# Kernel tuning notes

Measured on AMD Instinct MI355X. Metric: run time of the kernel, lower is better.

Reference implementation:

```python
import jax, jax.numpy as jnp
import numpy as np

D_IN = 2048
D_OUT = 2048
NUM_HEADS = 32
NUM_KV_GROUPS = 8
HEAD_DIM = D_OUT // NUM_HEADS          # 64
GROUP_SIZE = NUM_HEADS // NUM_KV_GROUPS  # 4
BATCH = 2
SEQ = 2048


def _rope(x, cos, sin):
    # x: [b, h, s, d]; cos/sin: [s, d]
    d = x.shape[-1]
    x1, x2 = x[..., : d // 2], x[..., d // 2:]
    rotated = jnp.concatenate((-x2, x1), axis=-1)
    return x * cos[None, None, :, :] + rotated * sin[None, None, :, :]


def setup_inputs() -> dict:
    key = jax.random.key(0)
    ks = jax.random.split(key, 8)
    x = jax.random.normal(ks[0], (BATCH, SEQ, D_IN), dtype=jnp.float32)
    cos = jax.random.normal(ks[1], (SEQ, HEAD_DIM), dtype=jnp.float32)
    sin = jax.random.normal(ks[2], (SEQ, HEAD_DIM), dtype=jnp.float32)
    # causal mask: True above the diagonal = masked out
    mask = jnp.triu(jnp.ones((SEQ, SEQ), dtype=jnp.bool_), k=1)
    s = 0.02
    Wq = jax.random.normal(ks[3], (D_IN, D_OUT), dtype=jnp.float32) * s
    Wk = jax.random.normal(ks[4], (D_IN, NUM_KV_GROUPS * HEAD_DIM), dtype=jnp.float32) * s
    Wv = jax.random.normal(ks[5], (D_IN, NUM_KV_GROUPS * HEAD_DIM), dtype=jnp.float32) * s
    Wo = jax.random.normal(ks[6], (D_OUT, D_OUT), dtype=jnp.float32) * s
    return {"x": x, "cos": cos, "sin": sin, "mask": mask,
            "Wq": Wq, "Wk": Wk, "Wv": Wv, "Wo": Wo}


def reference(x, cos, sin, mask, Wq, Wk, Wv, Wo):
    b, s, _ = x.shape
    # projections (Linear, no bias): weights stored as [d_in, d_out]
    q = (x @ Wq).reshape(b, s, NUM_HEADS, HEAD_DIM).transpose(0, 2, 1, 3)      # [b,H,s,d]
    k = (x @ Wk).reshape(b, s, NUM_KV_GROUPS, HEAD_DIM).transpose(0, 2, 1, 3)  # [b,G,s,d]
    v = (x @ Wv).reshape(b, s, NUM_KV_GROUPS, HEAD_DIM).transpose(0, 2, 1, 3)  # [b,G,s,d]
    q = _rope(q, cos, sin)
    k = _rope(k, cos, sin)
    # GQA broadcast: repeat each KV group group_size times along head axis
    k = jnp.repeat(k, GROUP_SIZE, axis=1)  # [b,H,s,d]
    v = jnp.repeat(v, GROUP_SIZE, axis=1)  # [b,H,s,d]
    scores = jnp.einsum('bhqd,bhkd->bhqk', q, k)
    scores = jnp.where(mask[None, None, :, :], -jnp.inf, scores)
    # original scales AFTER masking: softmax(scores / sqrt(head_dim)); -inf stays -inf
    attn = jax.nn.softmax(scores * (1.0 / np.sqrt(HEAD_DIM)), axis=-1)
    ctx = jnp.einsum('bhqk,bhkd->bqhd', attn, v).reshape(b, s, D_OUT)
    return ctx @ Wo
```

## Files before the change

### kernel.cpp

```cpp
#include <hip/hip_runtime.h>
#include <hip/hip_fp16.h>

#define SEQ    2048
#define DIN    2048
#define DOUT   2048
#define NH     32
#define NKV    8
#define HD     64
#define BB     2
#define NT_K   32

typedef _Float16 half_t;
typedef __attribute__((ext_vector_type(8))) _Float16 half8;
typedef __attribute__((ext_vector_type(4))) _Float16 half4;
typedef __attribute__((ext_vector_type(2))) __fp16   fp16x2;
typedef __attribute__((ext_vector_type(4))) float    floatx4;

union H8U { half8 h; int u[4]; };
union H2I { fp16x2 h; int i; };

#if __has_builtin(__builtin_amdgcn_exp2f)
#define EXP2F(x) __builtin_amdgcn_exp2f(x)
#else
#define EXP2F(x) __expf((x) * 0.6931471805599453f)
#endif

__device__ __forceinline__ void gload16(void* l, const void* g) {
    __builtin_amdgcn_global_load_lds(
        (const __attribute__((address_space(1))) void*)g,
        (__attribute__((address_space(3))) void*)l, 16, 0, 0);
}

__device__ __forceinline__ void phase_bar() {
    __builtin_amdgcn_sched_barrier(0);
    __builtin_amdgcn_s_barrier();
    __builtin_amdgcn_sched_barrier(0);
}
#define LGKM0() do { asm volatile("s_waitcnt lgkmcnt(0)" ::: "memory"); \
                     __builtin_amdgcn_sched_barrier(0); } while (0)
#define VMW(n)  do { asm volatile("s_waitcnt vmcnt(" #n ")" ::: "memory"); \
                     __builtin_amdgcn_sched_barrier(0); } while (0)

__global__ void cast_f2h(const float* __restrict__ in, half_t* __restrict__ out, int n4) {
    int i = blockIdx.x * blockDim.x + threadIdx.x;
    if (i < n4) {
        float4 v = ((const float4*)in)[i];
        half4 h;
        h[0] = (half_t)v.x; h[1] = (half_t)v.y; h[2] = (half_t)v.z; h[3] = (half_t)v.w;
        ((half4*)out)[i] = h;
    }
}

__global__ __launch_bounds__(256) void tcast(const float* __restrict__ in, half_t* __restrict__ out,
                                             int Kd, int Nd) {
    __shared__ float T[32][33];
    int x0 = blockIdx.x * 32, y0 = blockIdx.y * 32;
    int tx = threadIdx.x & 31, ty = threadIdx.x >> 5;
    #pragma unroll
    for (int j = 0; j < 4; j++)
        T[ty + j * 8][tx] = in[(size_t)(y0 + ty + j * 8) * Nd + x0 + tx];
    __syncthreads();
    #pragma unroll
    for (int j = 0; j < 4; j++)
        out[(size_t)(x0 + ty + j * 8) * Kd + y0 + tx] = (half_t)T[tx][ty + j * 8];
}

__device__ __forceinline__ void gemm256_core(
    const half_t* __restrict__ A, const half_t* __restrict__ Bt,
    int m0, int n0, half_t* As, half_t* Bs, floatx4 (&acc)[8][4])
{
    const int tid  = threadIdx.x;
    const int wave = tid >> 6, lane = tid & 63;
    const int quad = lane >> 4, l15 = lane & 15;
    const int wr128 = (wave >> 2) * 128, wc64 = (wave & 3) * 64;
    const int K = DIN;

    const half_t* pa[4]; const half_t* pb[4]; int ldso[4];
    #pragma unroll
    for (int is = 0; is < 4; is++) {
        int s  = is * 512 + tid;
        int kb = s >> 10, s1 = s & 1023;
        int p  = s1 >> 3, c = (s1 & 7) ^ (p & 7);
        int row  = 2 * p + (c >> 2);
        int koff = kb * 32 + (c & 3) * 8;
        pa[is] = A  + (size_t)(m0 + row) * K + koff;
        pb[is] = Bt + (size_t)(n0 + row) * K + koff;
        ldso[is] = (is * 512 + wave * 64) * 8;
    }
    int aoff[8], boff[4];
    #pragma unroll
    for (int m = 0; m < 8; m++) {
        int r = wr128 + m * 16 + l15, p = r >> 1;
        aoff[m] = p * 64 + ((((r & 1) * 4 + quad) ^ (p & 7)) * 8);
    }
    #pragma unroll
    for (int n = 0; n < 4; n++) {
        int r = wc64 + n * 16 + l15, p = r >> 1;
        boff[n] = p * 64 + ((((r & 1) * 4 + quad) ^ (p & 7)) * 8);
    }

    #pragma unroll
    for (int is = 0; is < 4; is++) {
        gload16(As + ldso[is], pa[is]);
        gload16(Bs + ldso[is], pb[is]);
    }
    #pragma unroll
    for (int is = 0; is < 4; is++) {
        gload16(As + 16384 + ldso[is], pa[is] + 64);
        gload16(Bs + 16384 + ldso[is], pb[is] + 64);
    }
    VMW(8);
    phase_bar();

    half8 af[4][2], bf[4][2];
    for (int T = 0; T < NT_K; T++) {
        half_t* cA = As + (T & 1) * 16384;
        half_t* cB = Bs + (T & 1) * 16384;

        #pragma unroll
        for (int mi = 0; mi < 4; mi++) {
            af[mi][0] = *(const half8*)(cA + aoff[mi]);
            af[mi][1] = *(const half8*)(cA + 8192 + aoff[mi]);
        }
        #pragma unroll
        for (int ni = 0; ni < 2; ni++) {
            bf[ni][0] = *(const half8*)(cB + boff[ni]);
            bf[ni][1] = *(const half8*)(cB + 8192 + boff[ni]);
        }
        phase_bar();
        LGKM0();
        __builtin_amdgcn_s_setprio(1);
        #pragma unroll
        for (int ni = 0; ni < 2; ni++)
            #pragma unroll
            for (int mi = 0; mi < 4; mi++)
                #pragma unroll
                for (int ks = 0; ks < 2; ks++)
                    acc[mi][ni] = __builtin_amdgcn_mfma_f32_16x16x32_f16(af[mi][ks], bf[ni][ks], acc[mi][ni], 0, 0, 0);
        __builtin_amdgcn_s_setprio(0);
        phase_bar();

        #pragma unroll
        for (int ni = 2; ni < 4; ni++) {
            bf[ni][0] = *(const half8*)(cB + boff[ni]);
            bf[ni][1] = *(const half8*)(cB + 8192 + boff[ni]);
        }
        phase_bar();
        LGKM0();
        __builtin_amdgcn_s_setprio(1);
        #pragma unroll
        for (int ni = 2; ni < 4; ni++)
            #pragma unroll
            for (int mi = 0; mi < 4; mi++)
                #pragma unroll
                for (int ks = 0; ks < 2; ks++)
                    acc[mi][ni] = __builtin_amdgcn_mfma_f32_16x16x32_f16(af[mi][ks], bf[ni][ks], acc[mi][ni], 0, 0, 0);
        __builtin_amdgcn_s_setprio(0);
        phase_bar();

        #pragma unroll
        for (int mi = 0; mi < 4; mi++) {
            af[mi][0] = *(const half8*)(cA + aoff[4 + mi]);
            af[mi][1] = *(const half8*)(cA + 8192 + aoff[4 + mi]);
        }
        phase_bar();
        LGKM0();
        __builtin_amdgcn_s_setprio(1);
        #pragma unroll
        for (int ni = 0; ni < 2; ni++)
            #pragma unroll
            for (int mi = 0; mi < 4; mi++)
                #pragma unroll
                for (int ks = 0; ks < 2; ks++)
                    acc[4 + mi][ni] = __builtin_amdgcn_mfma_f32_16x16x32_f16(af[mi][ks], bf[ni][ks], acc[4 + mi][ni], 0, 0, 0);
        __builtin_amdgcn_s_setprio(0);
        phase_bar();

        if (T + 2 < NT_K) {
            const int kk = (T + 2) * 64;
            #pragma unroll
            for (int is = 0; is < 4; is++) {
                gload16(cA + ldso[is], pa[is] + kk);
                gload16(cB + ldso[is], pb[is] + kk);
            }
            __builtin_amdgcn_s_setprio(1);
            #pragma unroll
            for (int ni = 2; ni < 4; ni++)
                #pragma unroll
                for (int mi = 0; mi < 4; mi++)
                    #pragma unroll
                    for (int ks = 0; ks < 2; ks++)
                        acc[4 + mi][ni] = __builtin_amdgcn_mfma_f32_16x16x32_f16(af[mi][ks], bf[ni][ks], acc[4 + mi][ni], 0, 0, 0);
            __builtin_amdgcn_s_setprio(0);
            VMW(8);
        } else {
            __builtin_amdgcn_s_setprio(1);
            #pragma unroll
            for (int ni = 2; ni < 4; ni++)
                #pragma unroll
                for (int mi = 0; mi < 4; mi++)
                    #pragma unroll
                    for (int ks = 0; ks < 2; ks++)
                        acc[4 + mi][ni] = __builtin_amdgcn_mfma_f32_16x16x32_f16(af[mi][ks], bf[ni][ks], acc[4 + mi][ni], 0, 0, 0);
            __builtin_amdgcn_s_setprio(0);
            VMW(0);
        }
        phase_bar();
    }
}

__global__ __launch_bounds__(512, 2) void gemm_qkv(
    const half_t* __restrict__ A, const half_t* __restrict__ Bt,
    const float* __restrict__ cosb, const float* __restrict__ sinb,
    half_t* __restrict__ Qh, half_t* __restrict__ Kh, half_t* __restrict__ Vt)
{
    __shared__ half_t As[2][16384];
    __shared__ half_t Bs[2][16384];
    const int m0 = blockIdx.y * 256, n0 = blockIdx.x * 256;

    floatx4 acc[8][4] = {};
    gemm256_core(A, Bt, m0, n0, &As[0][0], &Bs[0][0], acc);

    const int tid = threadIdx.x, wave = tid >> 6, lane = tid & 63;
    const int quad = lane >> 4, l15 = lane & 15;
    const int wr128 = (wave >> 2) * 128, wc64 = (wave & 3) * 64;
    const int headg = (n0 + wc64) >> 6;
    const int b = m0 >> 11;
    const int s_base = (m0 & 2047) + wr128 + quad * 4;

    if (headg < 32) {
        half_t* outp = Qh + (size_t)(b * NH + headg) * SEQ * 64;
        #pragma unroll
        for (int m = 0; m < 8; m++)
            #pragma unroll
            for (int n = 0; n < 4; n++) {
                int d = n * 16 + l15;
                #pragma unroll
                for (int r = 0; r < 4; r++)
                    outp[(size_t)(s_base + m * 16 + r) * 64 + d] = (half_t)acc[m][n][r];
            }
    } else if (headg < 40) {
        half_t* outp = Kh + (size_t)(b * NKV + (headg - 32)) * SEQ * 64;
        #pragma unroll
        for (int m = 0; m < 8; m++)
            #pragma unroll
            for (int r = 0; r < 4; r++) {
                int s = s_base + m * 16 + r;
                #pragma unroll
                for (int j = 0; j < 2; j++) {
                    int d = j * 16 + l15;
                    float x1 = acc[m][j][r], x2 = acc[m][j + 2][r];
                    float c1 = cosb[s * 64 + d],      s1 = sinb[s * 64 + d];
                    float c2 = cosb[s * 64 + d + 32], s2 = sinb[s * 64 + d + 32];
                    outp[(size_t)s * 64 + d]      = (half_t)(x1 * c1 - x2 * s1);
                    outp[(size_t)s * 64 + d + 32] = (half_t)(x2 * c2 + x1 * s2);
                }
            }
    } else {
        half_t* vtp = Vt + (size_t)(b * NKV + (headg - 40)) * 64 * SEQ;
        #pragma unroll
        for (int m = 0; m < 8; m++) {
            int s = s_base + m * 16;
            #pragma unroll
            for (int n = 0; n < 4; n++) {
                int d = n * 16 + l15;
                half4 hv;
                hv[0] = (half_t)acc[m][n][0];
                hv[1] = (half_t)acc[m][n][1];
                hv[2] = (half_t)acc[m][n][2];
                hv[3] = (half_t)acc[m][n][3];
                *(half4*)(vtp + (size_t)d * SEQ + s) = hv;
            }
        }
    }
}

__global__ __launch_bounds__(512, 2) void gemm_tn_f(
    const half_t* __restrict__ A, const half_t* __restrict__ Bt,
    float* __restrict__ C)
{
    __shared__ half_t As[2][16384];
    __shared__ half_t Bs[2][16384];
    const int m0 = blockIdx.y * 256, n0 = blockIdx.x * 256;

    floatx4 acc[8][4] = {};
    gemm256_core(A, Bt, m0, n0, &As[0][0], &Bs[0][0], acc);

    const int tid = threadIdx.x, wave = tid >> 6, lane = tid & 63;
    const int quad = lane >> 4, l15 = lane & 15;
    const int wr128 = (wave >> 2) * 128, wc64 = (wave & 3) * 64;
    #pragma unroll
    for (int m = 0; m < 8; m++) {
        int row = m0 + wr128 + m * 16 + quad * 4;
        #pragma unroll
        for (int n = 0; n < 4; n++) {
            int col = n0 + wc64 + n * 16 + l15;
            #pragma unroll
            for (int r = 0; r < 4; r++)
                C[(size_t)(row + r) * DOUT + col] = acc[m][n][r];
        }
    }
}

__global__ __launch_bounds__(256, 4) void attn(
    const half_t* __restrict__ Qh, const half_t* __restrict__ Kh,
    const half_t* __restrict__ Vt, const float* __restrict__ cosb,
    const float* __restrict__ sinb, half_t* __restrict__ ctx)
{
    __shared__ half_t Ks[2][4096];
    __shared__ half_t Vs[2][4096];

    const int tid = threadIdx.x, wave = tid >> 6, lane = tid & 63;
    const int quad = lane >> 4, l15 = lane & 15;
    const int bid = blockIdx.x;
    const int k  = bid >> 8;
    const int u  = bid & 255;
    const int q2 = u & 3;
    const int bh = u >> 2;
    const int qt = (k == 0) ? 15 - 2 * q2 : (k == 1) ? 2 * q2
                 : (k == 2) ? 14 - 2 * q2 : 2 * q2 + 1;
    const int b  = bh >> 5;
    const int h  = bh & 31;
    const int g  = h >> 2;
    const int q0 = qt * 128;
    const int wm = wave * 32;

    const half_t* kp = Kh + (size_t)(b * NKV + g) * SEQ * 64;
    const half_t* vp = Vt + (size_t)(b * NKV + g) * 64 * SEQ;

    half8 qf[2][2];
    {
        const float sc = 0.125f * 1.44269504088896f;
        const half_t* qpp = Qh + ((size_t)(b * NH + h) * SEQ + q0 + wm) * 64;
        #pragma unroll
        for (int mf = 0; mf < 2; mf++) {
            int s = q0 + wm + mf * 16 + l15;
            const float* cp = cosb + s * 64 + quad * 8;
            const float* sp = sinb + s * 64 + quad * 8;
            half8 xa = *(const half8*)(qpp + (size_t)(mf * 16 + l15) * 64 + quad * 8);
            half8 xb = *(const half8*)(qpp + (size_t)(mf * 16 + l15) * 64 + 32 + quad * 8);
            float4 c1a = *(const float4*)(cp),      c1b = *(const float4*)(cp + 4);
            float4 s1a = *(const float4*)(sp),      s1b = *(const float4*)(sp + 4);
            float4 c2a = *(const float4*)(cp + 32), c2b = *(const float4*)(cp + 36);
            float4 s2a = *(const float4*)(sp + 32), s2b = *(const float4*)(sp + 36);
            #pragma unroll
            for (int t = 0; t < 8; t++) {
                float cc1 = (t < 4) ? ((const float*)&c1a)[t] : ((const float*)&c1b)[t - 4];
                float ss1 = (t < 4) ? ((const float*)&s1a)[t] : ((const float*)&s1b)[t - 4];
                float cc2 = (t < 4) ? ((const float*)&c2a)[t] : ((const float*)&c2b)[t - 4];
                float ss2 = (t < 4) ? ((const float*)&s2a)[t] : ((const float*)&s2b)[t - 4];
                float x1 = (float)xa[t], x2 = (float)xb[t];
                qf[mf][0][t] = (half_t)((x1 * cc1 - x2 * ss1) * sc);
                qf[mf][1][t] = (half_t)((x2 * cc2 + x1 * ss2) * sc);
            }
        }
    }

    int koff[2], voff[2], lo[2];
    #pragma unroll
    for (int is = 0; is < 2; is++) {
        int s = is * 256 + tid;
        int p = s >> 3, c = (s & 7) ^ (p & 7);
        koff[is] = p * 64 + c * 8;
        voff[is] = p * SEQ + c * 8;
        lo[is]   = (is * 256 + wave * 64) * 8;
    }

    float m_i[2], l_i[2];
    m_i[0] = m_i[1] = -__builtin_inff();
    l_i[0] = l_i[1] = 0.f;
    floatx4 o[2][4] = {};

    const int ntiles = 2 * qt + 2;
    #pragma unroll
    for (int is = 0; is < 2; is++) {
        gload16(&Ks[0][lo[is]], kp + koff[is]);
        gload16(&Vs[0][lo[is]], vp + voff[is]);
    }

    const int srcA = l15 + ((quad & 1) ? 32 : 0);
    const int srcB = srcA + 16;
    const bool hiK = (quad >> 1) != 0;

    for (int kt = 0; kt < ntiles; kt++) {
        const int cur = kt & 1;
        const int kb  = kt * 64;
        __syncthreads();
        if (kt + 1 < ntiles) {
            const int kb2 = (kt + 1) * 64;
            #pragma unroll
            for (int is = 0; is < 2; is++) {
                gload16(&Ks[cur ^ 1][lo[is]], kp + (size_t)kb2 * 64 + koff[is]);
                gload16(&Vs[cur ^ 1][lo[is]], vp + kb2 + voff[is]);
            }
        }

        if (kb <= q0 + wm + 31) {
            floatx4 sa[2][4] = {};
            #pragma unroll
            for (int kc = 0; kc < 2; kc++)
                #pragma unroll
                for (int kf = 0; kf < 4; kf++) {
                    int row = kf * 16 + l15;
                    int sc = ((kc * 4 + quad) ^ (row & 7));
                    half8 kfr = *(const half8*)&Ks[cur][row * 64 + sc * 8];
                    sa[0][kf] = __builtin_amdgcn_mfma_f32_16x16x32_f16(kfr, qf[0][kc], sa[0][kf], 0, 0, 0);
                    sa[1][kf] = __builtin_amdgcn_mfma_f32_16x16x32_f16(kfr, qf[1][kc], sa[1][kf], 0, 0, 0);
                }

            if (kb + 63 > q0 + wm) {
                #pragma unroll
                for (int kf = 0; kf < 4; kf++)
                    #pragma unroll
                    for (int r = 0; r < 4; r++) {
                        int key = kb + kf * 16 + quad * 4 + r;
                        if (key > q0 + wm + l15)      sa[0][kf][r] = -__builtin_inff();
                        if (key > q0 + wm + 16 + l15) sa[1][kf][r] = -__builtin_inff();
                    }
            }

            int eh[2][4][2];
            float alpha[2];
            #pragma unroll
            for (int mf = 0; mf < 2; mf++) {
                float mt = sa[mf][0][0];
                #pragma unroll
                for (int kf = 0; kf < 4; kf++)
                    #pragma unroll
                    for (int r = 0; r < 4; r++) mt = fmaxf(mt, sa[mf][kf][r]);
                mt = fmaxf(mt, __shfl_xor(mt, 16));
                mt = fmaxf(mt, __shfl_xor(mt, 32));
                float mn = fmaxf(m_i[mf], mt);
                alpha[mf] = EXP2F(m_i[mf] - mn);
                m_i[mf] = mn;
                float rs = 0.f;
                #pragma unroll
                for (int kf = 0; kf < 4; kf++) {
                    float e0 = EXP2F(sa[mf][kf][0] - mn);
                    float e1 = EXP2F(sa[mf][kf][1] - mn);
                    float e2 = EXP2F(sa[mf][kf][2] - mn);
                    float e3 = EXP2F(sa[mf][kf][3] - mn);
                    rs += (e0 + e1) + (e2 + e3);
                    H2I p01, p23;
                    p01.h = __builtin_amdgcn_cvt_pkrtz(e0, e1);
                    p23.h = __builtin_amdgcn_cvt_pkrtz(e2, e3);
                    eh[mf][kf][0] = p01.i;
                    eh[mf][kf][1] = p23.i;
                }
                rs += __shfl_xor(rs, 16);
                rs += __shfl_xor(rs, 32);
                l_i[mf] = l_i[mf] * alpha[mf] + rs;
                #pragma unroll
                for (int nf = 0; nf < 4; nf++)
                    #pragma unroll
                    for (int r = 0; r < 4; r++) o[mf][nf][r] *= alpha[mf];
            }

            #pragma unroll
            for (int kc = 0; kc < 2; kc++) {
                H8U pf[2];
                #pragma unroll
                for (int mf = 0; mf < 2; mf++) {
                    int a0 = __shfl(eh[mf][2 * kc][0],     srcA);
                    int a1 = __shfl(eh[mf][2 * kc][1],     srcA);
                    int b0 = __shfl(eh[mf][2 * kc + 1][0], srcA);
                    int b1 = __shfl(eh[mf][2 * kc + 1][1], srcA);
                    int c0 = __shfl(eh[mf][2 * kc][0],     srcB);
                    int c1 = __shfl(eh[mf][2 * kc][1],     srcB);
                    int d0 = __shfl(eh[mf][2 * kc + 1][0], srcB);
                    int d1 = __shfl(eh[mf][2 * kc + 1][1], srcB);
                    pf[mf].u[0] = hiK ? b0 : a0;
                    pf[mf].u[1] = hiK ? b1 : a1;
                    pf[mf].u[2] = hiK ? d0 : c0;
                    pf[mf].u[3] = hiK ? d1 : c1;
                }
                #pragma unroll
                for (int nf = 0; nf < 4; nf++) {
                    int row = nf * 16 + l15;
                    int sc = ((kc * 4 + quad) ^ (row & 7));
                    half8 vf = *(const half8*)&Vs[cur][row * 64 + sc * 8];
                    o[0][nf] = __builtin_amdgcn_mfma_f32_16x16x32_f16(vf, pf[0].h, o[0][nf], 0, 0, 0);
                    o[1][nf] = __builtin_amdgcn_mfma_f32_16x16x32_f16(vf, pf[1].h, o[1][nf], 0, 0, 0);
                }
            }
        }
    }

    #pragma unroll
    for (int mf = 0; mf < 2; mf++) {
        float inv = 1.0f / l_i[mf];
        int s = q0 + wm + mf * 16 + l15;
        half_t* op = ctx + (size_t)(b * SEQ + s) * DOUT + h * 64 + quad * 4;
        #pragma unroll
        for (int nf = 0; nf < 4; nf++) {
            half4 hv;
            hv[0] = (half_t)(o[mf][nf][0] * inv);
            hv[1] = (half_t)(o[mf][nf][1] * inv);
            hv[2] = (half_t)(o[mf][nf][2] * inv);
            hv[3] = (half_t)(o[mf][nf][3] * inv);
            *(half4*)(op + nf * 16) = hv;
        }
    }
}

extern "C" void kernel_launch(void* const* d_in, const int* in_sizes, int n_in,
                              void* d_out, int out_size, void* d_ws, size_t ws_size,
                              hipStream_t stream) {
    const float* x    = (const float*)d_in[0];
    const float* cosb = (const float*)d_in[1];
    const float* sinb = (const float*)d_in[2];
    const float* Wq   = (const float*)d_in[4];
    const float* Wk   = (const float*)d_in[5];
    const float* Wv   = (const float*)d_in[6];
    const float* Wo   = (const float*)d_in[7];
    float* out = (float*)d_out;

    const size_t M  = (size_t)BB * SEQ;
    const size_t nX = M * DIN;

    char* ws = (char*)d_ws;
    const size_t MB = 1048576;
    half_t* xh     = (half_t*)(ws);
    half_t* WqkvT  = (half_t*)(ws + 16 * MB);
    half_t* WoT    = (half_t*)(ws + 28 * MB);
    half_t* Qh     = (half_t*)(ws + 36 * MB);
    half_t* Kh     = (half_t*)(ws + 52 * MB);
    half_t* Vt     = (half_t*)(ws + 56 * MB);
    half_t* ctxh   = (half_t*)(ws + 60 * MB);

    cast_f2h<<<(nX / 4) / 256, 256, 0, stream>>>(x, xh, nX / 4);
    tcast<<<dim3(64, 64), 256, 0, stream>>>(Wq, WqkvT, DIN, DOUT);
    tcast<<<dim3(16, 64), 256, 0, stream>>>(Wk, WqkvT + (size_t)2048 * 2048, DIN, 512);
    tcast<<<dim3(16, 64), 256, 0, stream>>>(Wv, WqkvT + (size_t)2560 * 2048, DIN, 512);
    tcast<<<dim3(64, 64), 256, 0, stream>>>(Wo, WoT, DOUT, DOUT);

    gemm_qkv<<<dim3(3072 / 256, M / 256), 512, 0, stream>>>(xh, WqkvT, cosb, sinb, Qh, Kh, Vt);

    attn<<<BB * NH * (SEQ / 128), 256, 0, stream>>>(Qh, Kh, Vt, cosb, sinb, ctxh);

    gemm_tn_f<<<dim3(DOUT / 256, M / 256), 512, 0, stream>>>(ctxh, WoT, out);
}
```

Measured before the change: 383.0 us.

## Interleave GEMM global-to-LDS staging across MFMA phases at quarter-tile granularity

Reworks the GEMM main loop so each K-tile's global-to-LDS loads are split into four quarter stages (two A halves, two B halves). Each stage is issued inside a different MFMA phase, and vmcnt is waited at a finer level (vmcnt(2)). The loop is unrolled by two with static buffer pointers, and the sched_barrier fences around barriers and waits are removed. The aim is to spread memory traffic evenly over compute and shorten the time spent waiting on loads. The cost is that correctness now depends on delicate buffer-reuse ordering, and the compiler has more freedom to reorder code across waits.

After: 354.6 us. 1.08x faster.

```diff
diff --git a/kernel.cpp b/kernel.cpp
--- a/kernel.cpp
+++ b/kernel.cpp
@@ -31,15 +31,10 @@
         (__attribute__((address_space(3))) void*)l, 16, 0, 0);
 }
 
-__device__ __forceinline__ void phase_bar() {
-    __builtin_amdgcn_sched_barrier(0);
-    __builtin_amdgcn_s_barrier();
-    __builtin_amdgcn_sched_barrier(0);
-}
-#define LGKM0() do { asm volatile("s_waitcnt lgkmcnt(0)" ::: "memory"); \
-                     __builtin_amdgcn_sched_barrier(0); } while (0)
-#define VMW(n)  do { asm volatile("s_waitcnt vmcnt(" #n ")" ::: "memory"); \
-                     __builtin_amdgcn_sched_barrier(0); } while (0)
+#define BAR()   __builtin_amdgcn_s_barrier()
+#define LGKM0() asm volatile("s_waitcnt lgkmcnt(0)")
+#define VMW2()  asm volatile("s_waitcnt vmcnt(2)" ::: "memory")
+#define VMW0()  asm volatile("s_waitcnt vmcnt(0)" ::: "memory")
 
 __global__ void cast_f2h(const float* __restrict__ in, half_t* __restrict__ out, int n4) {
     int i = blockIdx.x * blockDim.x + threadIdx.x;
@@ -65,9 +60,39 @@
         out[(size_t)(x0 + ty + j * 8) * Kd + y0 + tx] = (half_t)T[tx][ty + j * 8];
 }
 
+#define DS_AQ(Q) \
+    _Pragma("unroll") \
+    for (int mi = 0; mi < 4; mi++) { \
+        af[mi][0] = *(const half8*)(cA + aoff[(Q) + mi]); \
+        af[mi][1] = *(const half8*)(cA + 8192 + aoff[(Q) + mi]); \
+    }
+#define DS_BH(N0, N1) \
+    _Pragma("unroll") \
+    for (int ni = (N0); ni < (N1); ni++) { \
+        bf[ni][0] = *(const half8*)(cB + boff[ni]); \
+        bf[ni][1] = *(const half8*)(cB + 8192 + boff[ni]); \
+    }
+#define MFMA_Q(MI0, NI0) \
+    __builtin_amdgcn_s_setprio(1); \
+    _Pragma("unroll") \
+    for (int ni = 0; ni < 2; ni++) \
+        _Pragma("unroll") \
+        for (int mi = 0; mi < 4; mi++) \
+            _Pragma("unroll") \
+            for (int ks = 0; ks < 2; ks++) \
+                acc[(MI0) + mi][(NI0) + ni] = __builtin_amdgcn_mfma_f32_16x16x32_f16( \
+                    af[mi][ks], bf[(NI0) + ni][ks], acc[(MI0) + mi][(NI0) + ni], 0, 0, 0); \
+    __builtin_amdgcn_s_setprio(0);
+
+#define PH_GROUP(STG0, STG1, STG2, STG3, VMW_) \
+    DS_AQ(0); DS_BH(0, 2); STG0; BAR(); LGKM0(); MFMA_Q(0, 0); BAR(); \
+    DS_BH(2, 4);           STG1; BAR(); LGKM0(); MFMA_Q(0, 2); BAR(); \
+    DS_AQ(4);              STG2; BAR(); LGKM0(); MFMA_Q(4, 0); BAR(); \
+    STG3; MFMA_Q(4, 2); VMW_; BAR();
+
 __device__ __forceinline__ void gemm256_core(
     const half_t* __restrict__ A, const half_t* __restrict__ Bt,
-    int m0, int n0, half_t* As, half_t* Bs, floatx4 (&acc)[8][4])
+    int m0, int n0, half_t* AsB, half_t* BsB, floatx4 (&acc)[8][4])
 {
     const int tid  = threadIdx.x;
     const int wave = tid >> 6, lane = tid & 63;
@@ -99,113 +124,47 @@
         boff[n] = p * 64 + ((((r & 1) * 4 + quad) ^ (p & 7)) * 8);
     }
 
-    #pragma unroll
-    for (int is = 0; is < 4; is++) {
-        gload16(As + ldso[is], pa[is]);
-        gload16(Bs + ldso[is], pb[is]);
-    }
-    #pragma unroll
-    for (int is = 0; is < 4; is++) {
-        gload16(As + 16384 + ldso[is], pa[is] + 64);
-        gload16(Bs + 16384 + ldso[is], pb[is] + 64);
-    }
-    VMW(8);
-    phase_bar();
+    auto stage = [&](int tile, int ht) {
+        const int kk = tile * 64;
+        half_t* dst = (ht < 2 ? AsB : BsB) + (tile & 1) * 16384;
+        const int i0 = (ht & 1) * 2;
+        if (ht < 2) {
+            gload16(dst + ldso[i0],     pa[i0] + kk);
+            gload16(dst + ldso[i0 + 1], pa[i0 + 1] + kk);
+        } else {
+            gload16(dst + ldso[i0],     pb[i0] + kk);
+            gload16(dst + ldso[i0 + 1], pb[i0 + 1] + kk);
+        }
+    };
+
+    stage(0, 0); stage(0, 1); stage(0, 2); stage(0, 3);
+    stage(1, 0);
+    VMW2();
+    BAR();
 
     half8 af[4][2], bf[4][2];
-    for (int T = 0; T < NT_K; T++) {
-        half_t* cA = As + (T & 1) * 16384;
-        half_t* cB = Bs + (T & 1) * 16384;
-
-        #pragma unroll
-        for (int mi = 0; mi < 4; mi++) {
-            af[mi][0] = *(const half8*)(cA + aoff[mi]);
-            af[mi][1] = *(const half8*)(cA + 8192 + aoff[mi]);
-        }
-        #pragma unroll
-        for (int ni = 0; ni < 2; ni++) {
-            bf[ni][0] = *(const half8*)(cB + boff[ni]);
-            bf[ni][1] = *(const half8*)(cB + 8192 + boff[ni]);
-        }
-        phase_bar();
-        LGKM0();
-        __builtin_amdgcn_s_setprio(1);
-        #pragma unroll
-        for (int ni = 0; ni < 2; ni++)
-            #pragma unroll
-            for (int mi = 0; mi < 4; mi++)
-                #pragma unroll
-                for (int ks = 0; ks < 2; ks++)
-                    acc[mi][ni] = __builtin_amdgcn_mfma_f32_16x16x32_f16(af[mi][ks], bf[ni][ks], acc[mi][ni], 0, 0, 0);
-        __builtin_amdgcn_s_setprio(0);
-        phase_bar();
-
-        #pragma unroll
-        for (int ni = 2; ni < 4; ni++) {
-            bf[ni][0] = *(const half8*)(cB + boff[ni]);
-            bf[ni][1] = *(const half8*)(cB + 8192 + boff[ni]);
-        }
-        phase_bar();
-        LGKM0();
-        __builtin_amdgcn_s_setprio(1);
-        #pragma unroll
-        for (int ni = 2; ni < 4; ni++)
-            #pragma unroll
-            for (int mi = 0; mi < 4; mi++)
-                #pragma unroll
-                for (int ks = 0; ks < 2; ks++)
-                    acc[mi][ni] = __builtin_amdgcn_mfma_f32_16x16x32_f16(af[mi][ks], bf[ni][ks], acc[mi][ni], 0, 0, 0);
-        __builtin_amdgcn_s_setprio(0);
-        phase_bar();
-
-        #pragma unroll
-        for (int mi = 0; mi < 4; mi++) {
-            af[mi][0] = *(const half8*)(cA + aoff[4 + mi]);
-            af[mi][1] = *(const half8*)(cA + 8192 + aoff[4 + mi]);
-        }
-        phase_bar();
-        LGKM0();
-        __builtin_amdgcn_s_setprio(1);
-        #pragma unroll
-        for (int ni = 0; ni < 2; ni++)
-            #pragma unroll
-            for (int mi = 0; mi < 4; mi++)
-                #pragma unroll
-                for (int ks = 0; ks < 2; ks++)
-                    acc[4 + mi][ni] = __builtin_amdgcn_mfma_f32_16x16x32_f16(af[mi][ks], bf[ni][ks], acc[4 + mi][ni], 0, 0, 0);
-        __builtin_amdgcn_s_setprio(0);
-        phase_bar();
-
-        if (T + 2 < NT_K) {
-            const int kk = (T + 2) * 64;
-            #pragma unroll
-            for (int is = 0; is < 4; is++) {
-                gload16(cA + ldso[is], pa[is] + kk);
-                gload16(cB + ldso[is], pb[is] + kk);
-            }
-            __builtin_amdgcn_s_setprio(1);
-            #pragma unroll
-            for (int ni = 2; ni < 4; ni++)
-                #pragma unroll
-                for (int mi = 0; mi < 4; mi++)
-                    #pragma unroll
-                    for (int ks = 0; ks < 2; ks++)
-                        acc[4 + mi][ni] = __builtin_amdgcn_mfma_f32_16x16x32_f16(af[mi][ks], bf[ni][ks], acc[4 + mi][ni], 0, 0, 0);
-            __builtin_amdgcn_s_setprio(0);
-            VMW(8);
-        } else {
-            __builtin_amdgcn_s_setprio(1);
-            #pragma unroll
-            for (int ni = 2; ni < 4; ni++)
-                #pragma unroll
-                for (int mi = 0; mi < 4; mi++)
-                    #pragma unroll
-                    for (int ks = 0; ks < 2; ks++)
-                        acc[4 + mi][ni] = __builtin_amdgcn_mfma_f32_16x16x32_f16(af[mi][ks], bf[ni][ks], acc[4 + mi][ni], 0, 0, 0);
-            __builtin_amdgcn_s_setprio(0);
-            VMW(0);
-        }
-        phase_bar();
+    #pragma unroll 1
+    for (int i = 0; i < NT_K / 2 - 1; i++) {
+        const int t0 = 2 * i;
+        {
+            const half_t* cA = AsB; const half_t* cB = BsB;
+            PH_GROUP(stage(t0 + 1, 1), stage(t0 + 1, 2), stage(t0 + 1, 3),
+                     stage(t0 + 2, 0), VMW2());
+        }
+        {
+            const half_t* cA = AsB + 16384; const half_t* cB = BsB + 16384;
+            PH_GROUP(stage(t0 + 2, 1), stage(t0 + 2, 2), stage(t0 + 2, 3),
+                     stage(t0 + 3, 0), VMW2());
+        }
+    }
+    {
+        const half_t* cA = AsB; const half_t* cB = BsB;
+        PH_GROUP(stage(NT_K - 1, 1), stage(NT_K - 1, 2), stage(NT_K - 1, 3),
+                 (void)0, VMW0());
+    }
+    {
+        const half_t* cA = AsB + 16384; const half_t* cB = BsB + 16384;
+        PH_GROUP((void)0, (void)0, (void)0, (void)0, (void)0);
     }
 }
 
```
